# Performance work log

Hardware: AMD Instinct MI355X
Metric: run time of the kernel (lower is better)

The kernel has to match this reference:

```python
import jax, jax.numpy as jnp
import numpy as np

VOCAB = 32000
FEAT = 1024
B, T = 16, 256


def setup_inputs() -> dict:
    key = jax.random.key(0)
    ks = jax.random.split(key, 12)
    s_in = 1.0 / np.sqrt(FEAT)
    inp = {
        "x": jax.random.randint(ks[0], (B, T), 0, VOCAB),
        "h0": jnp.zeros((2, B, FEAT), jnp.float32),
        "emb": jax.random.normal(ks[1], (VOCAB, FEAT), jnp.float32) * 0.02,
        "W_ih0": jax.random.uniform(ks[2], (3 * FEAT, FEAT), jnp.float32, -s_in, s_in),
        "W_hh0": jax.random.uniform(ks[3], (3 * FEAT, FEAT), jnp.float32, -s_in, s_in),
        "b_ih0": jax.random.uniform(ks[4], (3 * FEAT,), jnp.float32, -s_in, s_in),
        "b_hh0": jax.random.uniform(ks[5], (3 * FEAT,), jnp.float32, -s_in, s_in),
        "W_ih1": jax.random.uniform(ks[6], (3 * FEAT, FEAT), jnp.float32, -s_in, s_in),
        "W_hh1": jax.random.uniform(ks[7], (3 * FEAT, FEAT), jnp.float32, -s_in, s_in),
        "b_ih1": jax.random.uniform(ks[8], (3 * FEAT,), jnp.float32, -s_in, s_in),
        "b_hh1": jax.random.uniform(ks[9], (3 * FEAT,), jnp.float32, -s_in, s_in),
        "dec_b": jnp.zeros((VOCAB,), jnp.float32),
    }
    return inp


def _gru_layer(xs, h0, W_ih, W_hh, b_ih, b_hh):
    # xs: [T, B, H_in]; h0: [B, H]. PyTorch gate order: r, z, n.
    x_proj = jnp.einsum('tbi,gi->tbg', xs, W_ih) + b_ih  # [T, B, 3H]

    def step(h, xp):
        hp = h @ W_hh.T + b_hh  # [B, 3H]
        xr, xz, xn = jnp.split(xp, 3, axis=-1)
        hr, hz, hn = jnp.split(hp, 3, axis=-1)
        r = jax.nn.sigmoid(xr + hr)
        z = jax.nn.sigmoid(xz + hz)
        n = jnp.tanh(xn + r * hn)
        h_new = (1.0 - z) * n + z * h
        return h_new, h_new

    h_last, ys = jax.lax.scan(step, h0, x_proj)
    return ys, h_last


def reference(x, h0, emb, W_ih0, W_hh0, b_ih0, b_hh0, W_ih1, W_hh1, b_ih1, b_hh1, dec_b):
    xs = emb[x]  # [B, T, H]
    xs = jnp.transpose(xs, (1, 0, 2))  # time-major [T, B, H]
    ys0, h_last0 = _gru_layer(xs, h0[0], W_ih0, W_hh0, b_ih0, b_hh0)
    ys1, h_last1 = _gru_layer(ys0, h0[1], W_ih1, W_hh1, b_ih1, b_hh1)
    out = jnp.transpose(ys1, (1, 0, 2))  # [B, T, H]
    logits = jnp.einsum('bth,vh->btv', out, emb) + dec_b  # tied decoder
    hidden = jnp.stack([h_last0, h_last1], axis=0)  # [2, B, H]
    return logits, hidden
```

## Files before the change

kernel.cpp:

```cpp
#include <hip/hip_runtime.h>
#include <math.h>

#define FEAT 1024
#define NB 16
#define NT 256
#define VOCAB 32000
#define G3 3072
#define NWG 256
#define FLAG_STRIDE 32
#define NGRP 8
#define GSZ 32

#define BK 32
#define LDH 40
#define SMEM_BYTES 75584

typedef float f4 __attribute__((ext_vector_type(4)));
typedef float f32x4 __attribute__((ext_vector_type(4)));
typedef _Float16 half4v __attribute__((ext_vector_type(4)));
typedef _Float16 half8v __attribute__((ext_vector_type(8)));

__global__ __launch_bounds__(256) void gather_kernel(const int* __restrict__ x,
                                                     const float* __restrict__ emb,
                                                     float* __restrict__ xs) {
    int row = blockIdx.x;
    int t = row >> 4;
    int b = row & 15;
    int tok = x[b * NT + t];
    const float4* src = (const float4*)(emb + (size_t)tok * FEAT);
    float4* dst = (float4*)(xs + (size_t)row * FEAT);
    dst[threadIdx.x] = src[threadIdx.x];
}

__device__ __forceinline__ void store_f32_sc(float* p, float v) {
    asm volatile("global_store_dword %0, %1, off sc0 sc1" :: "v"(p), "v"(v) : "memory");
}
__device__ __forceinline__ void bar_arrive(unsigned* flag, unsigned expected) {
    asm volatile("s_waitcnt vmcnt(0)\n\t"
                 "global_store_dword %0, %1, off sc0 sc1"
                 :: "v"(flag), "v"(expected) : "memory");
}
__device__ __forceinline__ void bar_poll(const unsigned* p, unsigned expected) {
    unsigned v; int spins = 0;
    while (true) {
        asm volatile("global_load_dword %0, %1, off sc0 sc1\n\t"
                     "s_waitcnt vmcnt(0)"
                     : "=&v"(v) : "v"(p) : "memory");
        if (v >= expected) break;
        if (++spins > (1 << 20)) break;
        __builtin_amdgcn_s_sleep(1);
    }
}

__device__ __forceinline__ void gemm_tile(char* smemraw,
        const float* __restrict__ A, const float* __restrict__ Bm,
        const float* __restrict__ bias, float* __restrict__ C,
        int N, int K, int m_t, int n_t, int perm) {
    _Float16* AhS = (_Float16*)smemraw;
    _Float16* AlS = AhS + 128 * LDH;
    _Float16* BhS = AlS + 128 * LDH;
    _Float16* BlS = BhS + 128 * LDH;

    int tid = threadIdx.x;
    int srow = tid >> 1;
    int shf = tid & 1;

    const float* aptr = A + (size_t)(m_t * 128 + srow) * K + shf * 16;
    const float* bptr = Bm + (size_t)(n_t * 128 + srow) * K + shf * 16;

    int wid = tid >> 6;
    int wr = wid >> 1, wc = wid & 1;
    int lane = tid & 63;
    int fr = lane & 15;
    int ke = lane >> 4;

    f32x4 acc[4][4];
#pragma unroll
    for (int i = 0; i < 4; i++)
#pragma unroll
        for (int j = 0; j < 4; j++) acc[i][j] = (f32x4){0.f, 0.f, 0.f, 0.f};

    float4 a4[4], b4[4];
#pragma unroll
    for (int q = 0; q < 4; q++) {
        a4[q] = *(const float4*)(aptr + q * 4);
        b4[q] = *(const float4*)(bptr + q * 4);
    }

    for (int k0 = 0; k0 < K; k0 += BK) {
        __syncthreads();
#pragma unroll
        for (int q = 0; q < 4; q++) {
            half4v hh, hl;
            hh.x = (_Float16)a4[q].x; hl.x = (_Float16)(a4[q].x - (float)hh.x);
            hh.y = (_Float16)a4[q].y; hl.y = (_Float16)(a4[q].y - (float)hh.y);
            hh.z = (_Float16)a4[q].z; hl.z = (_Float16)(a4[q].z - (float)hh.z);
            hh.w = (_Float16)a4[q].w; hl.w = (_Float16)(a4[q].w - (float)hh.w);
            int o = srow * LDH + shf * 16 + q * 4;
            *(half4v*)&AhS[o] = hh;
            *(half4v*)&AlS[o] = hl;
            half4v gh, gl;
            gh.x = (_Float16)b4[q].x; gl.x = (_Float16)(b4[q].x - (float)gh.x);
            gh.y = (_Float16)b4[q].y; gl.y = (_Float16)(b4[q].y - (float)gh.y);
            gh.z = (_Float16)b4[q].z; gl.z = (_Float16)(b4[q].z - (float)gh.z);
            gh.w = (_Float16)b4[q].w; gl.w = (_Float16)(b4[q].w - (float)gh.w);
            *(half4v*)&BhS[o] = gh;
            *(half4v*)&BlS[o] = gl;
        }
        __syncthreads();

        if (k0 + BK < K) {
#pragma unroll
            for (int q = 0; q < 4; q++) {
                a4[q] = *(const float4*)(aptr + k0 + BK + q * 4);
                b4[q] = *(const float4*)(bptr + k0 + BK + q * 4);
            }
        }

        half8v ah[4], al[4], bh[4], bl[4];
#pragma unroll
        for (int i = 0; i < 4; i++) {
            int ao = (wr * 64 + i * 16 + fr) * LDH + ke * 8;
            ah[i] = *(const half8v*)&AhS[ao];
            al[i] = *(const half8v*)&AlS[ao];
            int bo = (wc * 64 + i * 16 + fr) * LDH + ke * 8;
            bh[i] = *(const half8v*)&BhS[bo];
            bl[i] = *(const half8v*)&BlS[bo];
        }
#pragma unroll
        for (int i = 0; i < 4; i++)
#pragma unroll
            for (int j = 0; j < 4; j++) {
                acc[i][j] = __builtin_amdgcn_mfma_f32_16x16x32_f16(ah[i], bh[j], acc[i][j], 0, 0, 0);
                acc[i][j] = __builtin_amdgcn_mfma_f32_16x16x32_f16(ah[i], bl[j], acc[i][j], 0, 0, 0);
                acc[i][j] = __builtin_amdgcn_mfma_f32_16x16x32_f16(al[i], bh[j], acc[i][j], 0, 0, 0);
            }
    }

#pragma unroll
    for (int j = 0; j < 4; j++) {
        int col = n_t * 128 + wc * 64 + j * 16 + fr;
        float bv = bias[col];
#pragma unroll
        for (int i = 0; i < 4; i++) {
#pragma unroll
            for (int v = 0; v < 4; v++) {
                int mrow = m_t * 128 + wr * 64 + i * 16 + 4 * ke + v;
                int orow = perm ? (((mrow & 15) << 8) | (mrow >> 4)) : mrow;
                C[(size_t)orow * N + col] = acc[i][j][v] + bv;
            }
        }
    }
}

__global__ __launch_bounds__(256, 2) void gemm_split16(
        const float* __restrict__ A, const float* __restrict__ Bm,
        const float* __restrict__ bias, float* __restrict__ C,
        int N, int K, int GM, int perm) {
    __shared__ __align__(16) char smem[4 * 128 * LDH * 2];
    int nNt = N >> 7;
    int perGroup = GM * nNt;
    int g = blockIdx.x / perGroup;
    int rix = blockIdx.x % perGroup;
    int n_t = rix / GM;
    int m_t = g * GM + (rix % GM);
    gemm_tile(smem, A, Bm, bias, C, N, K, m_t, n_t, perm);
}

__device__ __forceinline__ void scan_layer(char* smemraw,
        const float* __restrict__ xp, const float* __restrict__ Whh,
        const float* __restrict__ bhh, const float* __restrict__ h0src,
        float* __restrict__ ys, float* __restrict__ hid,
        unsigned* __restrict__ flags, unsigned* __restrict__ gflags) {
    float* w_lds   = (float*)smemraw;
    float* red     = w_lds + 12 * 1024;
    float* sums    = red + 192 * 33;
    float* bhh_lds = sums + 256;

    int wg = blockIdx.x;
    int j0 = wg * 4;
    int tid = threadIdx.x;

    for (int rr = 0; rr < 12; rr++) {
        int gate = rr >> 2, jloc = rr & 3;
        int grow = gate * FEAT + j0 + jloc;
        float4 v = ((const float4*)(Whh + (size_t)grow * FEAT))[tid];
        *(float4*)(w_lds + rr * 1024 + tid * 4) = v;
    }
    if (tid < 12) {
        int gate = tid >> 2, jloc = tid & 3;
        bhh_lds[tid] = bhh[gate * FEAT + j0 + jloc];
    }
    __syncthreads();

    int bg = tid >> 6;
    int kc = tid & 63;
    int pb = tid >> 2, pjl = tid & 3, pj = j0 + pjl;

    float xr = 0.f, xz = 0.f, xnv = 0.f, hreg = 0.f;
    if (tid < 64) {
        const float* xpr = xp + (size_t)(0 * NB + pb) * G3;
        xr = xpr[pj]; xz = xpr[FEAT + pj]; xnv = xpr[2 * FEAT + pj];
        hreg = h0src[pb * FEAT + pj];
    }

    for (int t = 0; t < NT; t++) {
        const float* hc = (t == 0) ? h0src : (ys + (size_t)(t - 1) * NB * FEAT);

        f4 h4[16];
#pragma unroll
        for (int bi = 0; bi < 4; bi++) {
            const float* hp = hc + (size_t)(bg * 4 + bi) * FEAT + kc * 4;
#pragma unroll
            for (int q = 0; q < 4; q++)
                h4[bi * 4 + q] = *(const f4*)(hp + q * 256);
        }

        float part[48];
#pragma unroll
        for (int i = 0; i < 48; i++) part[i] = 0.f;
#pragma unroll
        for (int q = 0; q < 4; q++) {
            int kof = q * 256 + kc * 4;
#pragma unroll
            for (int rr = 0; rr < 12; rr++) {
                f4 w = *(const f4*)&w_lds[rr * 1024 + kof];
#pragma unroll
                for (int bi = 0; bi < 4; bi++) {
                    f4 h = h4[bi * 4 + q];
                    float p = part[rr * 4 + bi];
                    p = fmaf(h.x, w.x, p); p = fmaf(h.y, w.y, p);
                    p = fmaf(h.z, w.z, p); p = fmaf(h.w, w.w, p);
                    part[rr * 4 + bi] = p;
                }
            }
        }
#pragma unroll
        for (int i = 0; i < 48; i++) part[i] += __shfl_xor(part[i], 1);
        if ((kc & 1) == 0) {
#pragma unroll
            for (int rr = 0; rr < 12; rr++)
#pragma unroll
                for (int bi = 0; bi < 4; bi++)
                    red[(rr * 16 + bg * 4 + bi) * 33 + (kc >> 1)] = part[rr * 4 + bi];
        }
        __syncthreads();

        if (tid < 192) {
            float s = 0.f;
#pragma unroll
            for (int c = 0; c < 32; c++) s += red[tid * 33 + c];
            sums[tid] = s;
        }
        __syncthreads();

        if (tid < 64) {
            float dr = sums[pjl * 16 + pb] + bhh_lds[pjl];
            float dz = sums[(4 + pjl) * 16 + pb] + bhh_lds[4 + pjl];
            float dn = sums[(8 + pjl) * 16 + pb] + bhh_lds[8 + pjl];
            float r = 1.f / (1.f + expf(-(xr + dr)));
            float z = 1.f / (1.f + expf(-(xz + dz)));
            float n = tanhf(xnv + r * dn);
            float hv = (1.f - z) * n + z * hreg;
            hreg = hv;
            store_f32_sc(ys + (size_t)(t * NB + pb) * FEAT + pj, hv);
            if (t == NT - 1) hid[pb * FEAT + pj] = hv;
        }

        unsigned expected = (unsigned)(t + 1);
        __syncthreads();
        if (tid == 0) bar_arrive(&flags[wg * FLAG_STRIDE], expected);
        if (tid < 64) {
            int tn = (t + 1 < NT) ? t + 1 : t;
            const float* xpr = xp + (size_t)(tn * NB + pb) * G3;
            xr = xpr[pj]; xz = xpr[FEAT + pj]; xnv = xpr[2 * FEAT + pj];
        }
        if (wg < NGRP) {
            if (tid < GSZ) bar_poll(flags + (wg * GSZ + tid) * FLAG_STRIDE, expected);
            if (tid == 0) {
                asm volatile("global_store_dword %0, %1, off sc0 sc1"
                             :: "v"(&gflags[wg * FLAG_STRIDE]), "v"(expected) : "memory");
            }
        }
        if (tid < NGRP) bar_poll(gflags + tid * FLAG_STRIDE, expected);
        __builtin_amdgcn_sched_barrier(0);
        __syncthreads();
    }
}

__global__ __launch_bounds__(256, 2) void phase1(
        const float* __restrict__ xp, const float* __restrict__ Whh0,
        const float* __restrict__ bhh0, const float* __restrict__ h0,
        float* __restrict__ ys0, float* __restrict__ hid,
        unsigned* __restrict__ flags0, unsigned* __restrict__ gflags0,
        const float* __restrict__ Wih1, const float* __restrict__ bih1,
        float* __restrict__ xpw) {
    __shared__ __align__(16) char smem[SMEM_BYTES];
    if (blockIdx.x < NWG) {
        scan_layer(smem, xp, Whh0, bhh0, h0, ys0, hid, flags0, gflags0);
    } else {
        int bid = blockIdx.x - NWG;
        int perGroup = 8 * (G3 >> 7);
        int g = bid / perGroup, rix = bid % perGroup;
        int n_t = rix / 8, m_t = g * 8 + (rix % 8);
        unsigned gate = (unsigned)((m_t + 1) * 8);
        if (threadIdx.x < NGRP) bar_poll(gflags0 + threadIdx.x * FLAG_STRIDE, gate);
        __builtin_amdgcn_sched_barrier(0);
        __syncthreads();
        gemm_tile(smem, ys0, Wih1, bih1, xpw, G3, FEAT, m_t, n_t, 0);
    }
}

__global__ __launch_bounds__(256, 2) void phase2(
        const float* __restrict__ xp, const float* __restrict__ Whh1,
        const float* __restrict__ bhh1, const float* __restrict__ h0b,
        float* __restrict__ ys1, float* __restrict__ hid1,
        unsigned* __restrict__ flags1, unsigned* __restrict__ gflags1,
        const float* __restrict__ emb, const float* __restrict__ dec_b,
        float* __restrict__ out) {
    __shared__ __align__(16) char smem[SMEM_BYTES];
    if (blockIdx.x < NWG) {
        scan_layer(smem, xp, Whh1, bhh1, h0b, ys1, hid1, flags1, gflags1);
    } else {
        int bid = blockIdx.x - NWG;
        int perGroup = 8 * (VOCAB >> 7);
        int g = bid / perGroup, rix = bid % perGroup;
        int n_t = rix / 8, m_t = g * 8 + (rix % 8);
        unsigned gate = (unsigned)((m_t + 1) * 8);
        if (threadIdx.x < NGRP) bar_poll(gflags1 + threadIdx.x * FLAG_STRIDE, gate);
        __builtin_amdgcn_sched_barrier(0);
        __syncthreads();
        gemm_tile(smem, ys1, emb, dec_b, out, VOCAB, FEAT, m_t, n_t, 1);
    }
}

extern "C" void kernel_launch(void* const* d_in, const int* in_sizes, int n_in,
                              void* d_out, int out_size, void* d_ws, size_t ws_size,
                              hipStream_t stream) {
    const int*   x     = (const int*)d_in[0];
    const float* h0    = (const float*)d_in[1];
    const float* emb   = (const float*)d_in[2];
    const float* W_ih0 = (const float*)d_in[3];
    const float* W_hh0 = (const float*)d_in[4];
    const float* b_ih0 = (const float*)d_in[5];
    const float* b_hh0 = (const float*)d_in[6];
    const float* W_ih1 = (const float*)d_in[7];
    const float* W_hh1 = (const float*)d_in[8];
    const float* b_ih1 = (const float*)d_in[9];
    const float* b_hh1 = (const float*)d_in[10];
    const float* dec_b = (const float*)d_in[11];

    float* out = (float*)d_out;
    float* hid_out = out + (size_t)NB * NT * VOCAB;

    float* ws  = (float*)d_ws;
    float* xp  = ws;
    float* xs  = xp + (size_t)4096 * 3072;
    float* ys0 = xs + (size_t)4096 * 1024;
    float* pad = ys0 + (size_t)4096 * 1024;
    unsigned* flags0  = (unsigned*)(pad + 2 * NB * FEAT);
    unsigned* gflags0 = flags0 + NWG * FLAG_STRIDE;
    unsigned* flags1  = gflags0 + NGRP * FLAG_STRIDE;
    unsigned* gflags1 = flags1 + NWG * FLAG_STRIDE;
    float* ys1 = xs;

    hipMemsetAsync((void*)flags0, 0,
                   (2 * NWG + 2 * NGRP) * FLAG_STRIDE * sizeof(unsigned), stream);

    gather_kernel<<<dim3(NT * NB), dim3(256), 0, stream>>>(x, emb, xs);

    gemm_split16<<<dim3((4096 / 128) * (G3 / 128)), dim3(256), 0, stream>>>(
        xs, W_ih0, b_ih0, xp, G3, FEAT, 8, 0);

    phase1<<<dim3(NWG + (4096 / 128) * (G3 / 128)), dim3(256), 0, stream>>>(
        xp, W_hh0, b_hh0, h0, ys0, hid_out, flags0, gflags0, W_ih1, b_ih1, xp);

    phase2<<<dim3(NWG + (4096 / 128) * (VOCAB / 128)), dim3(256), 0, stream>>>(
        xp, W_hh1, b_hh1, h0 + NB * FEAT, ys1, hid_out + NB * FEAT,
        flags1, gflags1, emb, dec_b, out);
}
```

Baseline: 3.625 ms.

## Fuse layer-0 input projection GEMM into scan kernel with per-tile readiness counters

Drops the separate layer-0 input-projection GEMM launch and runs those tiles as extra workgroups inside phase1. Each tile stores its results coherently and bumps a per-row-block atomic counter. The scan waits on that counter before reading the xp rows for the next 8 timesteps, so the recurrence can start as soon as the first row block is ready instead of after the whole GEMM. Scan workgroups also raise their wave priority. The xp loads now happen at the start of each step instead of being prefetched during the barrier, which may add latency on the serial critical path and extra polling.

```diff
diff --git a/kernel.cpp b/kernel.cpp
--- a/kernel.cpp
+++ b/kernel.cpp
@@ -10,6 +10,7 @@
 #define FLAG_STRIDE 32
 #define NGRP 8
 #define GSZ 32
+#define NXPT 24
 
 #define BK 32
 #define LDH 40
@@ -55,7 +56,8 @@
 __device__ __forceinline__ void gemm_tile(char* smemraw,
         const float* __restrict__ A, const float* __restrict__ Bm,
         const float* __restrict__ bias, float* __restrict__ C,
-        int N, int K, int m_t, int n_t, int perm) {
+        int N, int K, int m_t, int n_t, int perm,
+        int coherent, unsigned* cnt) {
     _Float16* AhS = (_Float16*)smemraw;
     _Float16* AlS = AhS + 128 * LDH;
     _Float16* BhS = AlS + 128 * LDH;
@@ -147,35 +149,32 @@
             for (int v = 0; v < 4; v++) {
                 int mrow = m_t * 128 + wr * 64 + i * 16 + 4 * ke + v;
                 int orow = perm ? (((mrow & 15) << 8) | (mrow >> 4)) : mrow;
-                C[(size_t)orow * N + col] = acc[i][j][v] + bv;
-            }
-        }
-    }
-}
-
-__global__ __launch_bounds__(256, 2) void gemm_split16(
-        const float* __restrict__ A, const float* __restrict__ Bm,
-        const float* __restrict__ bias, float* __restrict__ C,
-        int N, int K, int GM, int perm) {
-    __shared__ __align__(16) char smem[4 * 128 * LDH * 2];
-    int nNt = N >> 7;
-    int perGroup = GM * nNt;
-    int g = blockIdx.x / perGroup;
-    int rix = blockIdx.x % perGroup;
-    int n_t = rix / GM;
-    int m_t = g * GM + (rix % GM);
-    gemm_tile(smem, A, Bm, bias, C, N, K, m_t, n_t, perm);
+                float val = acc[i][j][v] + bv;
+                if (coherent) store_f32_sc(&C[(size_t)orow * N + col], val);
+                else          C[(size_t)orow * N + col] = val;
+            }
+        }
+    }
+    if (cnt) {
+        asm volatile("s_waitcnt vmcnt(0)" ::: "memory");
+        __syncthreads();
+        if (tid == 0)
+            __hip_atomic_fetch_add(cnt, 1u, __ATOMIC_RELAXED, __HIP_MEMORY_SCOPE_AGENT);
+    }
 }
 
 __device__ __forceinline__ void scan_layer(char* smemraw,
         const float* __restrict__ xp, const float* __restrict__ Whh,
         const float* __restrict__ bhh, const float* __restrict__ h0src,
         float* __restrict__ ys, float* __restrict__ hid,
-        unsigned* __restrict__ flags, unsigned* __restrict__ gflags) {
+        unsigned* __restrict__ flags, unsigned* __restrict__ gflags,
+        const unsigned* __restrict__ xpcnt) {
     float* w_lds   = (float*)smemraw;
     float* red     = w_lds + 12 * 1024;
     float* sums    = red + 192 * 33;
     float* bhh_lds = sums + 256;
+
+    __builtin_amdgcn_s_setprio(1);
 
     int wg = blockIdx.x;
     int j0 = wg * 4;
@@ -191,22 +190,24 @@
         int gate = tid >> 2, jloc = tid & 3;
         bhh_lds[tid] = bhh[gate * FEAT + j0 + jloc];
     }
+    if (xpcnt && tid == 0) bar_poll(&xpcnt[0], NXPT);
     __syncthreads();
 
     int bg = tid >> 6;
     int kc = tid & 63;
     int pb = tid >> 2, pjl = tid & 3, pj = j0 + pjl;
 
-    float xr = 0.f, xz = 0.f, xnv = 0.f, hreg = 0.f;
-    if (tid < 64) {
-        const float* xpr = xp + (size_t)(0 * NB + pb) * G3;
-        xr = xpr[pj]; xz = xpr[FEAT + pj]; xnv = xpr[2 * FEAT + pj];
-        hreg = h0src[pb * FEAT + pj];
-    }
+    float hreg = 0.f;
+    if (tid < 64) hreg = h0src[pb * FEAT + pj];
 
     for (int t = 0; t < NT; t++) {
+        float xr = 0.f, xz = 0.f, xnv = 0.f;
+        if (tid < 64) {
+            const float* xpr = xp + (size_t)(t * NB + pb) * G3;
+            xr = xpr[pj]; xz = xpr[FEAT + pj]; xnv = xpr[2 * FEAT + pj];
+        }
+
         const float* hc = (t == 0) ? h0src : (ys + (size_t)(t - 1) * NB * FEAT);
-
         f4 h4[16];
 #pragma unroll
         for (int bi = 0; bi < 4; bi++) {
@@ -269,11 +270,12 @@
 
         unsigned expected = (unsigned)(t + 1);
         __syncthreads();
-        if (tid == 0) bar_arrive(&flags[wg * FLAG_STRIDE], expected);
-        if (tid < 64) {
-            int tn = (t + 1 < NT) ? t + 1 : t;
-            const float* xpr = xp + (size_t)(tn * NB + pb) * G3;
-            xr = xpr[pj]; xz = xpr[FEAT + pj]; xnv = xpr[2 * FEAT + pj];
+        if (tid == 0) {
+            bar_arrive(&flags[wg * FLAG_STRIDE], expected);
+            if (xpcnt) {
+                int nx = (t + 1 < NT) ? (t + 1) : (NT - 1);
+                bar_poll(&xpcnt[(nx >> 3) * FLAG_STRIDE], NXPT);
+            }
         }
         if (wg < NGRP) {
             if (tid < GSZ) bar_poll(flags + (wg * GSZ + tid) * FLAG_STRIDE, expected);
@@ -289,25 +291,35 @@
 }
 
 __global__ __launch_bounds__(256, 2) void phase1(
-        const float* __restrict__ xp, const float* __restrict__ Whh0,
+        float* __restrict__ xp, const float* __restrict__ Whh0,
         const float* __restrict__ bhh0, const float* __restrict__ h0,
         float* __restrict__ ys0, float* __restrict__ hid,
         unsigned* __restrict__ flags0, unsigned* __restrict__ gflags0,
-        const float* __restrict__ Wih1, const float* __restrict__ bih1,
-        float* __restrict__ xpw) {
+        const float* __restrict__ xs,
+        const float* __restrict__ Wih0, const float* __restrict__ bih0,
+        unsigned* __restrict__ xpcnt,
+        const float* __restrict__ Wih1, const float* __restrict__ bih1) {
     __shared__ __align__(16) char smem[SMEM_BYTES];
-    if (blockIdx.x < NWG) {
-        scan_layer(smem, xp, Whh0, bhh0, h0, ys0, hid, flags0, gflags0);
+    int bid = blockIdx.x;
+    if (bid < NWG) {
+        scan_layer(smem, xp, Whh0, bhh0, h0, ys0, hid, flags0, gflags0, xpcnt);
+    } else if (bid < NWG + (4096 / 128) * NXPT) {
+        int b2 = bid - NWG;
+        int perGroup = 8 * NXPT;
+        int g = b2 / perGroup, rix = b2 % perGroup;
+        int n_t = rix / 8, m_t = g * 8 + (rix % 8);
+        gemm_tile(smem, xs, Wih0, bih0, xp, G3, FEAT, m_t, n_t, 0,
+                  1, &xpcnt[m_t * FLAG_STRIDE]);
     } else {
-        int bid = blockIdx.x - NWG;
-        int perGroup = 8 * (G3 >> 7);
-        int g = bid / perGroup, rix = bid % perGroup;
+        int b2 = bid - NWG - (4096 / 128) * NXPT;
+        int perGroup = 8 * NXPT;
+        int g = b2 / perGroup, rix = b2 % perGroup;
         int n_t = rix / 8, m_t = g * 8 + (rix % 8);
         unsigned gate = (unsigned)((m_t + 1) * 8);
         if (threadIdx.x < NGRP) bar_poll(gflags0 + threadIdx.x * FLAG_STRIDE, gate);
         __builtin_amdgcn_sched_barrier(0);
         __syncthreads();
-        gemm_tile(smem, ys0, Wih1, bih1, xpw, G3, FEAT, m_t, n_t, 0);
+        gemm_tile(smem, ys0, Wih1, bih1, xp, G3, FEAT, m_t, n_t, 0, 0, nullptr);
     }
 }
 
@@ -320,7 +332,7 @@
         float* __restrict__ out) {
     __shared__ __align__(16) char smem[SMEM_BYTES];
     if (blockIdx.x < NWG) {
-        scan_layer(smem, xp, Whh1, bhh1, h0b, ys1, hid1, flags1, gflags1);
+        scan_layer(smem, xp, Whh1, bhh1, h0b, ys1, hid1, flags1, gflags1, nullptr);
     } else {
         int bid = blockIdx.x - NWG;
         int perGroup = 8 * (VOCAB >> 7);
@@ -330,7 +342,7 @@
         if (threadIdx.x < NGRP) bar_poll(gflags1 + threadIdx.x * FLAG_STRIDE, gate);
         __builtin_amdgcn_sched_barrier(0);
         __syncthreads();
-        gemm_tile(smem, ys1, emb, dec_b, out, VOCAB, FEAT, m_t, n_t, 1);
+        gemm_tile(smem, ys1, emb, dec_b, out, VOCAB, FEAT, m_t, n_t, 1, 0, nullptr);
     }
 }
 
@@ -362,18 +374,18 @@
     unsigned* gflags0 = flags0 + NWG * FLAG_STRIDE;
     unsigned* flags1  = gflags0 + NGRP * FLAG_STRIDE;
     unsigned* gflags1 = flags1 + NWG * FLAG_STRIDE;
+    unsigned* xpcnt   = gflags1 + NGRP * FLAG_STRIDE;
     float* ys1 = xs;
 
     hipMemsetAsync((void*)flags0, 0,
-                   (2 * NWG + 2 * NGRP) * FLAG_STRIDE * sizeof(unsigned), stream);
+                   (2 * NWG + 2 * NGRP + 32) * FLAG_STRIDE * sizeof(unsigned),
+                   stream);
 
     gather_kernel<<<dim3(NT * NB), dim3(256), 0, stream>>>(x, emb, xs);
 
-    gemm_split16<<<dim3((4096 / 128) * (G3 / 128)), dim3(256), 0, stream>>>(
-        xs, W_ih0, b_ih0, xp, G3, FEAT, 8, 0);
-
-    phase1<<<dim3(NWG + (4096 / 128) * (G3 / 128)), dim3(256), 0, stream>>>(
-        xp, W_hh0, b_hh0, h0, ys0, hid_out, flags0, gflags0, W_ih1, b_ih1, xp);
+    phase1<<<dim3(NWG + 2 * (4096 / 128) * NXPT), dim3(256), 0, stream>>>(
+        xp, W_hh0, b_hh0, h0, ys0, hid_out, flags0, gflags0,
+        xs, W_ih0, b_ih0, xpcnt, W_ih1, b_ih1);
 
     phase2<<<dim3(NWG + (4096 / 128) * (VOCAB / 128)), dim3(256), 0, stream>>>(
         xp, W_hh1, b_hh1, h0 + NB * FEAT, ys1, hid_out + NB * FEAT,
```

Result: no change. 3.679 ms (+1.5%).
